# Kernel optimization log

Measured on AMD Instinct MI355X. Metric: run time of the kernel, lower is better.

The kernel has to match this reference:

```python
import jax, jax.numpy as jnp
import numpy as np

RADIUS = 1.0      # cfg['radius']
NEAR = 0.5        # cfg['near']
N_STEPS = 32      # cfg['ray_marching_steps']
N_SECANT = 8      # n_secant_steps in unisurf()
TAU = 0.5         # occupancy decision threshold
EPS = 1e-6        # module-level epsilon


def _occ(p, W1, b1, W2, b2):
    # stand-in occupancy network: [..., 3] -> [...]
    h = jax.nn.relu(p @ W1 + b1)
    return jax.nn.sigmoid(h @ W2 + b2)[..., 0]


def get_sphere_intersection(cam_loc, rays, r=RADIUS):
    # cam_loc: [B,3], rays: [B,P,3] (unit). Faithful to the torch version.
    ray_cam_dot = jnp.einsum('bpd,bd->bp', rays, cam_loc)                    # [B,P]
    under_sqrt = ray_cam_dot ** 2 - (jnp.sum(cam_loc ** 2, -1, keepdims=True) - r * r)
    mask_intersect = under_sqrt > 0
    s = jnp.sqrt(jnp.where(mask_intersect, under_sqrt, 0.0))
    inter = jnp.stack([-s - ray_cam_dot, s - ray_cam_dot], axis=-1)          # [B,P,2]
    inter = jnp.where(mask_intersect[..., None], inter, 0.0)
    return jnp.maximum(inter, 0.0), mask_intersect


def setup_inputs() -> dict:
    key = jax.random.key(0)
    k1, k2, k3, k4, k5, k6 = jax.random.split(key, 6)
    B, P, H = 1, 131072, 32
    # camera ~2 units from origin; rays aimed at points near the unit sphere
    cam_loc = jnp.array([[0.0, 0.0, 2.0]], dtype=jnp.float32) + 0.01 * jax.random.normal(k1, (B, 3))
    targets = 0.3 * jax.random.normal(k2, (B, P, 3))
    ray_directions = (targets - cam_loc[:, None, :]).astype(jnp.float32)
    W1 = (0.8 * jax.random.normal(k3, (3, H))).astype(jnp.float32)
    b1 = (0.1 * jax.random.normal(k4, (H,))).astype(jnp.float32)
    W2 = (0.5 * jax.random.normal(k5, (H, 1))).astype(jnp.float32)
    b2 = (0.1 * jax.random.normal(k6, (1,))).astype(jnp.float32)
    return {"cam_loc": cam_loc, "ray_directions": ray_directions,
            "W1": W1, "b1": b1, "W2": W2, "b2": b2}


def reference(cam_loc, ray_directions, W1, b1, W2, b2):
    rays = ray_directions / jnp.linalg.norm(ray_directions, axis=-1, keepdims=True)
    inter, mask_int = get_sphere_intersection(cam_loc, rays, RADIUS)
    far = jnp.maximum(inter[..., 1], NEAR + EPS)                             # [B,P]

    # coarse march: N_STEPS samples per ray between near and sphere-far
    t = jnp.linspace(0.0, 1.0, N_STEPS, dtype=jnp.float32)                   # [S]
    d = NEAR * (1.0 - t) + far[..., None] * t                                # [B,P,S]
    p = cam_loc[:, None, None, :] + rays[:, :, None, :] * d[..., None]       # [B,P,S,3]
    f = _occ(p, W1, b1, W2, b2) - TAU                                        # [B,P,S]

    # first free->occupied sign change (masked-index pattern, vectorized)
    cross = (f[..., :-1] < 0) & (f[..., 1:] >= 0)                            # [B,P,S-1]
    found = jnp.any(cross, axis=-1) & mask_int                               # [B,P]
    idx = jnp.argmax(cross, axis=-1)                                         # [B,P]

    def take(a, i):
        return jnp.take_along_axis(a, i[..., None], axis=-1)[..., 0]

    d_low, f_low = take(d, idx), take(f, idx)
    d_high, f_high = take(d, idx + 1), take(f, idx + 1)

    def secant_body(_, c):
        dl, fl, dh, fh = c
        den = fh - fl
        den = jnp.where(jnp.abs(den) < EPS, EPS, den)
        dm = dl - fl * (dh - dl) / den
        pm = cam_loc[:, None, :] + rays * dm[..., None]
        fm = _occ(pm, W1, b1, W2, b2) - TAU
        neg = fm < 0
        return (jnp.where(neg, dm, dl), jnp.where(neg, fm, fl),
                jnp.where(neg, dh, dm), jnp.where(neg, fh, fm))

    d_low, f_low, d_high, f_high = jax.lax.fori_loop(
        0, N_SECANT, secant_body, (d_low, f_low, d_high, f_high))
    den = f_high - f_low
    den = jnp.where(jnp.abs(den) < EPS, EPS, den)
    d_mid = d_low - f_low * (d_high - d_low) / den
    d_pred = jnp.where(found, d_mid, 0.0)                                    # [B,P]

    # surface points fed back to the model (depth detached, as in torch)
    p_surf = cam_loc[:, None, :] + rays * jax.lax.stop_gradient(d_pred)[..., None]
    occ_surf = jnp.where(found, _occ(p_surf, W1, b1, W2, b2), 0.0)           # [B,P]
    return d_pred, occ_surf
```

## Files before the change

### kernel.cpp

```cpp
#include <hip/hip_runtime.h>
#include <math.h>

#define HDIM 32
#define NSTEPS 32
#define NSECANT 8
#define RADIUSV 1.0f
#define NEARV 0.5f
#define TAUV 0.5f
#define EPSV 1e-6f

typedef float f2 __attribute__((ext_vector_type(2)));

__global__ __launch_bounds__(256, 2) void unisurf_kernel(
    const float* __restrict__ cam_loc,
    const float* __restrict__ ray_dirs,
    const float* __restrict__ W1,
    const float* __restrict__ b1,
    const float* __restrict__ W2,
    const float* __restrict__ b2,
    float* __restrict__ out,
    int P)
{
    __shared__ float4 sW[HDIM];
    __shared__ float  sW2[HDIM];
    __shared__ float  sB2;

    const int tid = threadIdx.x;
    if (tid < HDIM) {
        sW[tid] = make_float4(W1[tid], W1[HDIM + tid], W1[2 * HDIM + tid], b1[tid]);
        sW2[tid] = W2[tid];
    }
    if (tid == 0) sB2 = b2[0];
    __syncthreads();

    const int r = blockIdx.x * blockDim.x + tid;
    if (r >= P) return;

    const float cx = cam_loc[0], cy = cam_loc[1], cz = cam_loc[2];

    float dx = ray_dirs[3 * r + 0];
    float dy = ray_dirs[3 * r + 1];
    float dz = ray_dirs[3 * r + 2];
    float nrm = sqrtf(dx * dx + dy * dy + dz * dz);
    float rx = dx / nrm, ry = dy / nrm, rz = dz / nrm;

    float rcd = rx * cx + ry * cy + rz * cz;
    float c2  = cx * cx + cy * cy + cz * cz;
    float us  = rcd * rcd - (c2 - RADIUSV * RADIUSV);
    bool  mask_int = us > 0.0f;
    float s_sq = mask_int ? sqrtf(us) : 0.0f;
    float far_raw = mask_int ? fmaxf(s_sq - rcd, 0.0f) : 0.0f;
    float farv = fmaxf(far_raw, NEARV + EPSV);

    f2 rW[HDIM / 2], cW[HDIM / 2], w2[HDIM / 2];
    #pragma unroll
    for (int h = 0; h < HDIM / 2; ++h) {
        float4 wa = sW[2 * h], wb = sW[2 * h + 1];
        rW[h] = (f2){rx * wa.x + ry * wa.y + rz * wa.z,
                     rx * wb.x + ry * wb.y + rz * wb.z};
        cW[h] = (f2){cx * wa.x + cy * wa.y + cz * wa.z + wa.w,
                     cx * wb.x + cy * wb.y + cz * wb.z + wb.w};
        w2[h] = (f2){sW2[2 * h], sW2[2 * h + 1]};
    }
    const float B2 = sB2;
    const f2 z2 = (f2){0.0f, 0.0f};

    auto logit2 = [&](float dA, float dB, float& lA, float& lB) {
        f2 dvA = (f2){dA, dA}, dvB = (f2){dB, dB};
        f2 aA0 = z2, aA1 = z2, aB0 = z2, aB1 = z2;
        #pragma unroll
        for (int h = 0; h < HDIM / 2; h += 2) {
            f2 xA0 = __builtin_elementwise_fma(dvA, rW[h + 0], cW[h + 0]);
            f2 xB0 = __builtin_elementwise_fma(dvB, rW[h + 0], cW[h + 0]);
            f2 xA1 = __builtin_elementwise_fma(dvA, rW[h + 1], cW[h + 1]);
            f2 xB1 = __builtin_elementwise_fma(dvB, rW[h + 1], cW[h + 1]);
            aA0 = __builtin_elementwise_fma(__builtin_elementwise_max(xA0, z2), w2[h + 0], aA0);
            aB0 = __builtin_elementwise_fma(__builtin_elementwise_max(xB0, z2), w2[h + 0], aB0);
            aA1 = __builtin_elementwise_fma(__builtin_elementwise_max(xA1, z2), w2[h + 1], aA1);
            aB1 = __builtin_elementwise_fma(__builtin_elementwise_max(xB1, z2), w2[h + 1], aB1);
        }
        f2 sA = aA0 + aA1, sB = aB0 + aB1;
        lA = (sA.x + sA.y) + B2;
        lB = (sB.x + sB.y) + B2;
    };
    auto logit = [&](float d) -> float {
        f2 dv = (f2){d, d};
        f2 a0 = z2, a1 = z2, a2 = z2, a3 = z2;
        #pragma unroll
        for (int h = 0; h < HDIM / 2; h += 4) {
            f2 x0 = __builtin_elementwise_fma(dv, rW[h + 0], cW[h + 0]);
            f2 x1 = __builtin_elementwise_fma(dv, rW[h + 1], cW[h + 1]);
            f2 x2 = __builtin_elementwise_fma(dv, rW[h + 2], cW[h + 2]);
            f2 x3 = __builtin_elementwise_fma(dv, rW[h + 3], cW[h + 3]);
            a0 = __builtin_elementwise_fma(__builtin_elementwise_max(x0, z2), w2[h + 0], a0);
            a1 = __builtin_elementwise_fma(__builtin_elementwise_max(x1, z2), w2[h + 1], a1);
            a2 = __builtin_elementwise_fma(__builtin_elementwise_max(x2, z2), w2[h + 2], a2);
            a3 = __builtin_elementwise_fma(__builtin_elementwise_max(x3, z2), w2[h + 3], a3);
        }
        f2 aa = (a0 + a1) + (a2 + a3);
        return (aa.x + aa.y) + B2;
    };
    auto sigm = [](float x) -> float {
        float e = __expf(-x);
        return __builtin_amdgcn_rcpf(1.0f + e);
    };

    const float STEPC = 0.03225806451612903f;

    unsigned msk = 0u;
    #pragma unroll 1
    for (int k = 0; k < 16; ++k) {
        float tA = (float)k * STEPC;
        float tB = (float)(k + 16) * STEPC;
        float dA = NEARV * (1.0f - tA) + farv * tA;
        float dB = NEARV * (1.0f - tB) + farv * tB;
        float lA, lB;
        logit2(dA, dB, lA, lB);
        unsigned bA = (lA >= 0.0f) ? (1u << k) : 0u;
        unsigned bB = (lB >= 0.0f) ? (1u << (k + 16)) : 0u;
        msk |= bA | bB;
    }

    unsigned cand = (~msk & (msk >> 1)) & 0x7FFFFFFFu;
    bool found = cand != 0u;
    int sstar = found ? __builtin_ctz(cand) : 0;
    found = found && mask_int;

    float tlo = (float)sstar * STEPC;
    float thi = (float)(sstar + 1) * STEPC;
    float d_lo = NEARV * (1.0f - tlo) + farv * tlo;
    float d_hi = NEARV * (1.0f - thi) + farv * thi;
    float lLo, lHi;
    logit2(d_lo, d_hi, lLo, lHi);
    float f_lo = sigm(lLo) - TAUV;
    float f_hi = sigm(lHi) - TAUV;

    #pragma unroll 1
    for (int it = 0; it < NSECANT; ++it) {
        float den = f_hi - f_lo;
        den = (fabsf(den) < EPSV) ? EPSV : den;
        float dm = d_lo - f_lo * (d_hi - d_lo) * __builtin_amdgcn_rcpf(den);
        float fm = sigm(logit(dm)) - TAUV;
        bool neg = fm < 0.0f;
        d_lo = neg ? dm : d_lo;
        f_lo = neg ? fm : f_lo;
        d_hi = neg ? d_hi : dm;
        f_hi = neg ? f_hi : fm;
    }
    float den = f_hi - f_lo;
    den = (fabsf(den) < EPSV) ? EPSV : den;
    float d_mid = d_lo - f_lo * (d_hi - d_lo) * __builtin_amdgcn_rcpf(den);

    float d_pred = found ? d_mid : 0.0f;
    float occ_s = sigm(logit(d_pred));
    float occ_surf = found ? occ_s : 0.0f;

    out[r]     = d_pred;
    out[P + r] = occ_surf;
}

extern "C" void kernel_launch(void* const* d_in, const int* in_sizes, int n_in,
                              void* d_out, int out_size, void* d_ws, size_t ws_size,
                              hipStream_t stream) {
    const float* cam_loc  = (const float*)d_in[0];
    const float* ray_dirs = (const float*)d_in[1];
    const float* W1       = (const float*)d_in[2];
    const float* b1       = (const float*)d_in[3];
    const float* W2       = (const float*)d_in[4];
    const float* b2       = (const float*)d_in[5];
    float* out = (float*)d_out;

    const int P = in_sizes[1] / 3;
    const int block = 256;
    const int grid = (P + block - 1) / block;
    unisurf_kernel<<<grid, block, 0, stream>>>(cam_loc, ray_dirs, W1, b1, W2, b2, out, P);
}
```

Measured before the change: 19.84 us.

## Run secant on logits, batch coarse march four-wide, precompute camera-weight terms

The secant search now operates directly on the network logit rather than sigmoid(logit)-0.5. Both share the same zero crossing, so the exp and reciprocal per evaluation are removed. The coarse march evaluates four samples per iteration instead of two, which gives more independent FMA chains and halves the loop trips. The camera-dependent hidden pre-activation is computed once per block in shared memory, and ray normalization uses a reciprocal square root. Interpolation on logits changes the intermediate secant points, so final depths may differ slightly from the reference, and the wider batch raises register pressure.

```diff
diff --git a/kernel.cpp b/kernel.cpp
--- a/kernel.cpp
+++ b/kernel.cpp
@@ -22,15 +22,19 @@
     int P)
 {
     __shared__ float4 sW[HDIM];
+    __shared__ float  sCW[HDIM];
     __shared__ float  sW2[HDIM];
     __shared__ float  sB2;
 
     const int tid = threadIdx.x;
     if (tid < HDIM) {
-        sW[tid] = make_float4(W1[tid], W1[HDIM + tid], W1[2 * HDIM + tid], b1[tid]);
+        float c0 = cam_loc[0], c1 = cam_loc[1], c2l = cam_loc[2];
+        float4 w4 = make_float4(W1[tid], W1[HDIM + tid], W1[2 * HDIM + tid], b1[tid]);
+        sW[tid] = w4;
+        sCW[tid] = c0 * w4.x + c1 * w4.y + c2l * w4.z + w4.w;
         sW2[tid] = W2[tid];
-    }
-    if (tid == 0) sB2 = b2[0];
+        if (tid == 0) sB2 = b2[0];
+    }
     __syncthreads();
 
     const int r = blockIdx.x * blockDim.x + tid;
@@ -41,8 +45,8 @@
     float dx = ray_dirs[3 * r + 0];
     float dy = ray_dirs[3 * r + 1];
     float dz = ray_dirs[3 * r + 2];
-    float nrm = sqrtf(dx * dx + dy * dy + dz * dz);
-    float rx = dx / nrm, ry = dy / nrm, rz = dz / nrm;
+    float inv = __builtin_amdgcn_rsqf(dx * dx + dy * dy + dz * dz);
+    float rx = dx * inv, ry = dy * inv, rz = dz * inv;
 
     float rcd = rx * cx + ry * cy + rz * cz;
     float c2  = cx * cx + cy * cy + cz * cz;
@@ -58,13 +62,43 @@
         float4 wa = sW[2 * h], wb = sW[2 * h + 1];
         rW[h] = (f2){rx * wa.x + ry * wa.y + rz * wa.z,
                      rx * wb.x + ry * wb.y + rz * wb.z};
-        cW[h] = (f2){cx * wa.x + cy * wa.y + cz * wa.z + wa.w,
-                     cx * wb.x + cy * wb.y + cz * wb.z + wb.w};
+        cW[h] = (f2){sCW[2 * h], sCW[2 * h + 1]};
         w2[h] = (f2){sW2[2 * h], sW2[2 * h + 1]};
     }
     const float B2 = sB2;
     const f2 z2 = (f2){0.0f, 0.0f};
 
+    auto logit4 = [&](float d0, float d1, float d2v, float d3,
+                      float& l0, float& l1, float& l2, float& l3) {
+        f2 dv0 = (f2){d0, d0}, dv1 = (f2){d1, d1};
+        f2 dv2 = (f2){d2v, d2v}, dv3 = (f2){d3, d3};
+        f2 a0a = z2, a0b = z2, a1a = z2, a1b = z2;
+        f2 a2a = z2, a2b = z2, a3a = z2, a3b = z2;
+        #pragma unroll
+        for (int h = 0; h < HDIM / 2; h += 2) {
+            f2 x0a = __builtin_elementwise_fma(dv0, rW[h + 0], cW[h + 0]);
+            f2 x1a = __builtin_elementwise_fma(dv1, rW[h + 0], cW[h + 0]);
+            f2 x2a = __builtin_elementwise_fma(dv2, rW[h + 0], cW[h + 0]);
+            f2 x3a = __builtin_elementwise_fma(dv3, rW[h + 0], cW[h + 0]);
+            f2 x0b = __builtin_elementwise_fma(dv0, rW[h + 1], cW[h + 1]);
+            f2 x1b = __builtin_elementwise_fma(dv1, rW[h + 1], cW[h + 1]);
+            f2 x2b = __builtin_elementwise_fma(dv2, rW[h + 1], cW[h + 1]);
+            f2 x3b = __builtin_elementwise_fma(dv3, rW[h + 1], cW[h + 1]);
+            a0a = __builtin_elementwise_fma(__builtin_elementwise_max(x0a, z2), w2[h + 0], a0a);
+            a1a = __builtin_elementwise_fma(__builtin_elementwise_max(x1a, z2), w2[h + 0], a1a);
+            a2a = __builtin_elementwise_fma(__builtin_elementwise_max(x2a, z2), w2[h + 0], a2a);
+            a3a = __builtin_elementwise_fma(__builtin_elementwise_max(x3a, z2), w2[h + 0], a3a);
+            a0b = __builtin_elementwise_fma(__builtin_elementwise_max(x0b, z2), w2[h + 1], a0b);
+            a1b = __builtin_elementwise_fma(__builtin_elementwise_max(x1b, z2), w2[h + 1], a1b);
+            a2b = __builtin_elementwise_fma(__builtin_elementwise_max(x2b, z2), w2[h + 1], a2b);
+            a3b = __builtin_elementwise_fma(__builtin_elementwise_max(x3b, z2), w2[h + 1], a3b);
+        }
+        f2 s0 = a0a + a0b, s1 = a1a + a1b, s2 = a2a + a2b, s3 = a3a + a3b;
+        l0 = (s0.x + s0.y) + B2;
+        l1 = (s1.x + s1.y) + B2;
+        l2 = (s2.x + s2.y) + B2;
+        l3 = (s3.x + s3.y) + B2;
+    };
     auto logit2 = [&](float dA, float dB, float& lA, float& lB) {
         f2 dvA = (f2){dA, dA}, dvB = (f2){dB, dB};
         f2 aA0 = z2, aA1 = z2, aB0 = z2, aB1 = z2;
@@ -109,16 +143,21 @@
 
     unsigned msk = 0u;
     #pragma unroll 1
-    for (int k = 0; k < 16; ++k) {
-        float tA = (float)k * STEPC;
-        float tB = (float)(k + 16) * STEPC;
-        float dA = NEARV * (1.0f - tA) + farv * tA;
-        float dB = NEARV * (1.0f - tB) + farv * tB;
-        float lA, lB;
-        logit2(dA, dB, lA, lB);
-        unsigned bA = (lA >= 0.0f) ? (1u << k) : 0u;
-        unsigned bB = (lB >= 0.0f) ? (1u << (k + 16)) : 0u;
-        msk |= bA | bB;
+    for (int k = 0; k < 8; ++k) {
+        float t0 = (float)k * STEPC;
+        float t1 = (float)(k + 8) * STEPC;
+        float t2 = (float)(k + 16) * STEPC;
+        float t3 = (float)(k + 24) * STEPC;
+        float dd0 = NEARV * (1.0f - t0) + farv * t0;
+        float dd1 = NEARV * (1.0f - t1) + farv * t1;
+        float dd2 = NEARV * (1.0f - t2) + farv * t2;
+        float dd3 = NEARV * (1.0f - t3) + farv * t3;
+        float l0, l1, l2, l3;
+        logit4(dd0, dd1, dd2, dd3, l0, l1, l2, l3);
+        msk |= (l0 >= 0.0f) ? (1u << k) : 0u;
+        msk |= (l1 >= 0.0f) ? (1u << (k + 8)) : 0u;
+        msk |= (l2 >= 0.0f) ? (1u << (k + 16)) : 0u;
+        msk |= (l3 >= 0.0f) ? (1u << (k + 24)) : 0u;
     }
 
     unsigned cand = (~msk & (msk >> 1)) & 0x7FFFFFFFu;
@@ -130,17 +169,15 @@
     float thi = (float)(sstar + 1) * STEPC;
     float d_lo = NEARV * (1.0f - tlo) + farv * tlo;
     float d_hi = NEARV * (1.0f - thi) + farv * thi;
-    float lLo, lHi;
-    logit2(d_lo, d_hi, lLo, lHi);
-    float f_lo = sigm(lLo) - TAUV;
-    float f_hi = sigm(lHi) - TAUV;
+    float f_lo, f_hi;
+    logit2(d_lo, d_hi, f_lo, f_hi);
 
     #pragma unroll 1
     for (int it = 0; it < NSECANT; ++it) {
         float den = f_hi - f_lo;
         den = (fabsf(den) < EPSV) ? EPSV : den;
         float dm = d_lo - f_lo * (d_hi - d_lo) * __builtin_amdgcn_rcpf(den);
-        float fm = sigm(logit(dm)) - TAUV;
+        float fm = logit(dm);
         bool neg = fm < 0.0f;
         d_lo = neg ? dm : d_lo;
         f_lo = neg ? fm : f_lo;
```

After: 19.30 us, median of 2. -2.7%, faster.

## Run coarse ray march in packed fp16, re-check near-threshold samples in fp32

Applied to the files above, without the earlier changes.

The 32-sample coarse march now evaluates the occupancy MLP with packed half-precision FMAs and fdot2 accumulation. Samples whose logit falls within a small margin of zero are recorded and re-evaluated in fp32 through a wave-uniform ballot loop, so that the sign decisions stay correct. The secant search now runs on raw logits instead of sigmoid minus tau, which drops the exponential per iteration but changes the interpolated depths. The camera-dependent layer-1 term is precomputed once per block, and the normalization uses rsq in place of sqrt plus divides.

```diff
diff --git a/kernel.cpp b/kernel.cpp
--- a/kernel.cpp
+++ b/kernel.cpp
@@ -8,8 +8,10 @@
 #define NEARV 0.5f
 #define TAUV 0.5f
 #define EPSV 1e-6f
+#define MARGINV 0.03f
 
 typedef float f2 __attribute__((ext_vector_type(2)));
+typedef _Float16 h2 __attribute__((ext_vector_type(2)));
 
 __global__ __launch_bounds__(256, 2) void unisurf_kernel(
     const float* __restrict__ cam_loc,
@@ -22,15 +24,19 @@
     int P)
 {
     __shared__ float4 sW[HDIM];
+    __shared__ float  sCW[HDIM];
     __shared__ float  sW2[HDIM];
     __shared__ float  sB2;
 
     const int tid = threadIdx.x;
     if (tid < HDIM) {
-        sW[tid] = make_float4(W1[tid], W1[HDIM + tid], W1[2 * HDIM + tid], b1[tid]);
+        float c0 = cam_loc[0], c1 = cam_loc[1], c2l = cam_loc[2];
+        float4 w4 = make_float4(W1[tid], W1[HDIM + tid], W1[2 * HDIM + tid], b1[tid]);
+        sW[tid] = w4;
+        sCW[tid] = c0 * w4.x + c1 * w4.y + c2l * w4.z + w4.w;
         sW2[tid] = W2[tid];
-    }
-    if (tid == 0) sB2 = b2[0];
+        if (tid == 0) sB2 = b2[0];
+    }
     __syncthreads();
 
     const int r = blockIdx.x * blockDim.x + tid;
@@ -41,8 +47,8 @@
     float dx = ray_dirs[3 * r + 0];
     float dy = ray_dirs[3 * r + 1];
     float dz = ray_dirs[3 * r + 2];
-    float nrm = sqrtf(dx * dx + dy * dy + dz * dz);
-    float rx = dx / nrm, ry = dy / nrm, rz = dz / nrm;
+    float inv = __builtin_amdgcn_rsqf(dx * dx + dy * dy + dz * dz);
+    float rx = dx * inv, ry = dy * inv, rz = dz * inv;
 
     float rcd = rx * cx + ry * cy + rz * cz;
     float c2  = cx * cx + cy * cy + cz * cz;
@@ -53,18 +59,40 @@
     float farv = fmaxf(far_raw, NEARV + EPSV);
 
     f2 rW[HDIM / 2], cW[HDIM / 2], w2[HDIM / 2];
+    h2 rWh[HDIM / 2], cWh[HDIM / 2], w2h[HDIM / 2];
     #pragma unroll
     for (int h = 0; h < HDIM / 2; ++h) {
         float4 wa = sW[2 * h], wb = sW[2 * h + 1];
         rW[h] = (f2){rx * wa.x + ry * wa.y + rz * wa.z,
                      rx * wb.x + ry * wb.y + rz * wb.z};
-        cW[h] = (f2){cx * wa.x + cy * wa.y + cz * wa.z + wa.w,
-                     cx * wb.x + cy * wb.y + cz * wb.z + wb.w};
+        cW[h] = (f2){sCW[2 * h], sCW[2 * h + 1]};
         w2[h] = (f2){sW2[2 * h], sW2[2 * h + 1]};
+        rWh[h] = (h2){(_Float16)rW[h].x, (_Float16)rW[h].y};
+        cWh[h] = (h2){(_Float16)cW[h].x, (_Float16)cW[h].y};
+        w2h[h] = (h2){(_Float16)w2[h].x, (_Float16)w2[h].y};
     }
     const float B2 = sB2;
     const f2 z2 = (f2){0.0f, 0.0f};
-
+    const h2 zh = (h2){(_Float16)0.0f, (_Float16)0.0f};
+
+    auto logit2h = [&](float dA, float dB, float& lA, float& lB) {
+        _Float16 hA = (_Float16)dA, hB = (_Float16)dB;
+        h2 dvA = (h2){hA, hA}, dvB = (h2){hB, hB};
+        float aA0 = 0.0f, aA1 = 0.0f, aB0 = 0.0f, aB1 = 0.0f;
+        #pragma unroll
+        for (int h = 0; h < HDIM / 2; h += 2) {
+            h2 xA0 = __builtin_elementwise_fma(dvA, rWh[h + 0], cWh[h + 0]);
+            h2 xB0 = __builtin_elementwise_fma(dvB, rWh[h + 0], cWh[h + 0]);
+            h2 xA1 = __builtin_elementwise_fma(dvA, rWh[h + 1], cWh[h + 1]);
+            h2 xB1 = __builtin_elementwise_fma(dvB, rWh[h + 1], cWh[h + 1]);
+            aA0 = __builtin_amdgcn_fdot2(__builtin_elementwise_max(xA0, zh), w2h[h + 0], aA0, false);
+            aB0 = __builtin_amdgcn_fdot2(__builtin_elementwise_max(xB0, zh), w2h[h + 0], aB0, false);
+            aA1 = __builtin_amdgcn_fdot2(__builtin_elementwise_max(xA1, zh), w2h[h + 1], aA1, false);
+            aB1 = __builtin_amdgcn_fdot2(__builtin_elementwise_max(xB1, zh), w2h[h + 1], aB1, false);
+        }
+        lA = (aA0 + aA1) + B2;
+        lB = (aB0 + aB1) + B2;
+    };
     auto logit2 = [&](float dA, float dB, float& lA, float& lB) {
         f2 dvA = (f2){dA, dA}, dvB = (f2){dB, dB};
         f2 aA0 = z2, aA1 = z2, aB0 = z2, aB1 = z2;
@@ -107,7 +135,7 @@
 
     const float STEPC = 0.03225806451612903f;
 
-    unsigned msk = 0u;
+    unsigned msk = 0u, amb = 0u;
     #pragma unroll 1
     for (int k = 0; k < 16; ++k) {
         float tA = (float)k * STEPC;
@@ -115,10 +143,23 @@
         float dA = NEARV * (1.0f - tA) + farv * tA;
         float dB = NEARV * (1.0f - tB) + farv * tB;
         float lA, lB;
-        logit2(dA, dB, lA, lB);
-        unsigned bA = (lA >= 0.0f) ? (1u << k) : 0u;
-        unsigned bB = (lB >= 0.0f) ? (1u << (k + 16)) : 0u;
-        msk |= bA | bB;
+        logit2h(dA, dB, lA, lB);
+        msk |= (lA >= 0.0f) ? (1u << k) : 0u;
+        msk |= (lB >= 0.0f) ? (1u << (k + 16)) : 0u;
+        amb |= (fabsf(lA) < MARGINV) ? (1u << k) : 0u;
+        amb |= (fabsf(lB) < MARGINV) ? (1u << (k + 16)) : 0u;
+    }
+
+    while (__builtin_amdgcn_ballot_w64(amb != 0u)) {
+        if (amb != 0u) {
+            int s = __builtin_ctz(amb);
+            amb &= amb - 1u;
+            float t = (float)s * STEPC;
+            float dd = NEARV * (1.0f - t) + farv * t;
+            float ls = logit(dd);
+            unsigned bit = 1u << s;
+            msk = (ls >= 0.0f) ? (msk | bit) : (msk & ~bit);
+        }
     }
 
     unsigned cand = (~msk & (msk >> 1)) & 0x7FFFFFFFu;
@@ -130,17 +171,15 @@
     float thi = (float)(sstar + 1) * STEPC;
     float d_lo = NEARV * (1.0f - tlo) + farv * tlo;
     float d_hi = NEARV * (1.0f - thi) + farv * thi;
-    float lLo, lHi;
-    logit2(d_lo, d_hi, lLo, lHi);
-    float f_lo = sigm(lLo) - TAUV;
-    float f_hi = sigm(lHi) - TAUV;
+    float f_lo, f_hi;
+    logit2(d_lo, d_hi, f_lo, f_hi);
 
     #pragma unroll 1
     for (int it = 0; it < NSECANT; ++it) {
         float den = f_hi - f_lo;
         den = (fabsf(den) < EPSV) ? EPSV : den;
         float dm = d_lo - f_lo * (d_hi - d_lo) * __builtin_amdgcn_rcpf(den);
-        float fm = sigm(logit(dm)) - TAUV;
+        float fm = logit(dm);
         bool neg = fm < 0.0f;
         d_lo = neg ? dm : d_lo;
         f_lo = neg ? fm : f_lo;
```

After: 25.46 us. 1.28x slower.

## Replace coarse march with piecewise-linear breakpoint scan via LDS prefix sums

Applied to the files above, without the earlier changes.

Replaces the 32-sample coarse march, which ran the full MLP at every step, with an analytic decomposition. Each hidden unit's ReLU is linear in the step index between breakpoints, so the kernel scatters per-unit slope and intercept changes into an LDS table indexed by breakpoint step, then prefix-sums them to get the logit at every step. The secant loop now works on raw logits instead of sigmoid(logit)-tau, and camera-dependent weights are precomputed once per block. The changes add 64KB of shared memory per block, which limits occupancy, plus LDS atomics and an extra barrier. Dropping the sigmoid changes the secant iterates, so outputs may differ numerically from the reference.

```diff
diff --git a/kernel.cpp b/kernel.cpp
--- a/kernel.cpp
+++ b/kernel.cpp
@@ -22,27 +22,39 @@
     int P)
 {
     __shared__ float4 sW[HDIM];
+    __shared__ float  sCW[HDIM];
     __shared__ float  sW2[HDIM];
     __shared__ float  sB2;
+    __shared__ float  sAB[NSTEPS][256][2];
 
     const int tid = threadIdx.x;
+
+    {
+        float4* p4 = (float4*)&sAB[0][0][0];
+        #pragma unroll
+        for (int i = 0; i < 16; ++i)
+            p4[tid + i * 256] = make_float4(0.f, 0.f, 0.f, 0.f);
+    }
     if (tid < HDIM) {
-        sW[tid] = make_float4(W1[tid], W1[HDIM + tid], W1[2 * HDIM + tid], b1[tid]);
+        float c0 = cam_loc[0], c1 = cam_loc[1], c2l = cam_loc[2];
+        float4 w4 = make_float4(W1[tid], W1[HDIM + tid], W1[2 * HDIM + tid], b1[tid]);
+        sW[tid] = w4;
+        sCW[tid] = c0 * w4.x + c1 * w4.y + c2l * w4.z + w4.w;
         sW2[tid] = W2[tid];
-    }
-    if (tid == 0) sB2 = b2[0];
+        if (tid == 0) sB2 = b2[0];
+    }
     __syncthreads();
 
     const int r = blockIdx.x * blockDim.x + tid;
-    if (r >= P) return;
+    const int rc = (r < P) ? r : (P - 1);
 
     const float cx = cam_loc[0], cy = cam_loc[1], cz = cam_loc[2];
 
-    float dx = ray_dirs[3 * r + 0];
-    float dy = ray_dirs[3 * r + 1];
-    float dz = ray_dirs[3 * r + 2];
-    float nrm = sqrtf(dx * dx + dy * dy + dz * dz);
-    float rx = dx / nrm, ry = dy / nrm, rz = dz / nrm;
+    float dx = ray_dirs[3 * rc + 0];
+    float dy = ray_dirs[3 * rc + 1];
+    float dz = ray_dirs[3 * rc + 2];
+    float inv = __builtin_amdgcn_rsqf(dx * dx + dy * dy + dz * dz);
+    float rx = dx * inv, ry = dy * inv, rz = dz * inv;
 
     float rcd = rx * cx + ry * cy + rz * cz;
     float c2  = cx * cx + cy * cy + cz * cz;
@@ -58,12 +70,62 @@
         float4 wa = sW[2 * h], wb = sW[2 * h + 1];
         rW[h] = (f2){rx * wa.x + ry * wa.y + rz * wa.z,
                      rx * wb.x + ry * wb.y + rz * wb.z};
-        cW[h] = (f2){cx * wa.x + cy * wa.y + cz * wa.z + wa.w,
-                     cx * wb.x + cy * wb.y + cz * wb.z + wb.w};
+        cW[h] = (f2){sCW[2 * h], sCW[2 * h + 1]};
         w2[h] = (f2){sW2[2 * h], sW2[2 * h + 1]};
     }
     const float B2 = sB2;
     const f2 z2 = (f2){0.0f, 0.0f};
+
+    const float STEPC = 0.03225806451612903f;
+
+    const float DD = (farv - NEARV) * STEPC;
+    float C0 = B2, C1 = 0.0f;
+    #pragma unroll
+    for (int h = 0; h < HDIM / 2; ++h) {
+        #pragma unroll
+        for (int e = 0; e < 2; ++e) {
+            float rw = e ? rW[h].y : rW[h].x;
+            float cw = e ? cW[h].y : cW[h].x;
+            float q  = e ? w2[h].y : w2[h].x;
+            float alpha = fmaf(NEARV, rw, cw);
+            float rho   = rw * DD;
+            float qa = q * alpha;
+            float qr = q * rho;
+            float sig = -alpha * __builtin_amdgcn_rcpf(rho);
+            float scl = fminf(fmaxf(sig, -1.0f), 33.0f);
+            int   k   = (int)ceilf(scl);
+            bool rpos = rho >= 0.0f;
+            bool fold = rpos ? (k <= 0) : (k >= 1);
+            bool inr  = (k >= 1) && (k <= 31);
+            float sbar = rpos ? 1.0f : -1.0f;
+            C0 += fold ? qa : 0.0f;
+            C1 += fold ? qr : 0.0f;
+            float av = inr ? sbar * qr : 0.0f;
+            float bv = inr ? sbar * qa : 0.0f;
+            int   ks = inr ? k : 1;
+            atomicAdd(&sAB[ks][tid][0], av);
+            atomicAdd(&sAB[ks][tid][1], bv);
+        }
+    }
+    __syncthreads();
+
+    unsigned msk = (C0 >= 0.0f) ? 1u : 0u;
+    float cc0 = C0, cc1 = C1;
+    float sf = 1.0f;
+    #pragma unroll
+    for (int s = 1; s < NSTEPS; ++s) {
+        float2 ab = *(const float2*)&sAB[s][tid][0];
+        cc1 += ab.x;
+        cc0 += ab.y;
+        float L = fmaf(cc1, sf, cc0);
+        msk |= (L >= 0.0f) ? (1u << s) : 0u;
+        sf += 1.0f;
+    }
+
+    unsigned cand = (~msk & (msk >> 1)) & 0x7FFFFFFFu;
+    bool found = cand != 0u;
+    int sstar = found ? __builtin_ctz(cand) : 0;
+    found = found && mask_int;
 
     auto logit2 = [&](float dA, float dB, float& lA, float& lB) {
         f2 dvA = (f2){dA, dA}, dvB = (f2){dB, dB};
@@ -105,42 +167,19 @@
         return __builtin_amdgcn_rcpf(1.0f + e);
     };
 
-    const float STEPC = 0.03225806451612903f;
-
-    unsigned msk = 0u;
-    #pragma unroll 1
-    for (int k = 0; k < 16; ++k) {
-        float tA = (float)k * STEPC;
-        float tB = (float)(k + 16) * STEPC;
-        float dA = NEARV * (1.0f - tA) + farv * tA;
-        float dB = NEARV * (1.0f - tB) + farv * tB;
-        float lA, lB;
-        logit2(dA, dB, lA, lB);
-        unsigned bA = (lA >= 0.0f) ? (1u << k) : 0u;
-        unsigned bB = (lB >= 0.0f) ? (1u << (k + 16)) : 0u;
-        msk |= bA | bB;
-    }
-
-    unsigned cand = (~msk & (msk >> 1)) & 0x7FFFFFFFu;
-    bool found = cand != 0u;
-    int sstar = found ? __builtin_ctz(cand) : 0;
-    found = found && mask_int;
-
     float tlo = (float)sstar * STEPC;
     float thi = (float)(sstar + 1) * STEPC;
     float d_lo = NEARV * (1.0f - tlo) + farv * tlo;
     float d_hi = NEARV * (1.0f - thi) + farv * thi;
-    float lLo, lHi;
-    logit2(d_lo, d_hi, lLo, lHi);
-    float f_lo = sigm(lLo) - TAUV;
-    float f_hi = sigm(lHi) - TAUV;
+    float f_lo, f_hi;
+    logit2(d_lo, d_hi, f_lo, f_hi);
 
     #pragma unroll 1
     for (int it = 0; it < NSECANT; ++it) {
         float den = f_hi - f_lo;
         den = (fabsf(den) < EPSV) ? EPSV : den;
         float dm = d_lo - f_lo * (d_hi - d_lo) * __builtin_amdgcn_rcpf(den);
-        float fm = sigm(logit(dm)) - TAUV;
+        float fm = logit(dm);
         bool neg = fm < 0.0f;
         d_lo = neg ? dm : d_lo;
         f_lo = neg ? fm : f_lo;
@@ -155,8 +194,10 @@
     float occ_s = sigm(logit(d_pred));
     float occ_surf = found ? occ_s : 0.0f;
 
-    out[r]     = d_pred;
-    out[P + r] = occ_surf;
+    if (r < P) {
+        out[r]     = d_pred;
+        out[P + r] = occ_surf;
+    }
 }
 
 extern "C" void kernel_launch(void* const* d_in, const int* in_sizes, int n_in,
```

Result: slower. 52.33 us (+163.8%).
